# Kernel tuning notes

Hardware: AMD Instinct MI355X
Metric: run time of the kernel (lower is better)

Reference implementation:

```python
import jax, jax.numpy as jnp
import numpy as np

B, K, D = 16384, 64, 128


def setup_inputs() -> dict:
    key = jax.random.key(0)
    kx, kc = jax.random.split(key)
    x = jax.random.normal(kx, (B, D), dtype=jnp.float32)
    centers = jax.random.uniform(kc, (K, D), dtype=jnp.float32)  # torch.rand init
    return {"x": x, "centers": centers}


def reference(x, centers):
    batch, dim = x.shape
    k = centers.shape[0]
    # pairwise squared distances, same math as sum((x - c)^2)
    diff = x[:, None, :] - centers[None, :, :]          # [B, K, D]
    dist_sq = jnp.sum(diff * diff, axis=-1)             # [B, K]
    expo = -0.5 * dist_sq
    # safe softmax over clusters (identical to max-subtracted exp/sum)
    resp = jax.nn.softmax(expo, axis=-1)                # [B, K]
    log_resp = jnp.log(jnp.clip(resp, 1e-8))
    # hard assignment and per-cluster statistics
    assign = jnp.argmin(dist_sq, axis=-1)               # [B] int
    onehot = jax.nn.one_hot(assign, k, dtype=x.dtype)   # [B, K]
    cluster_weight = jnp.sum(onehot, axis=0)            # [K]
    emp_total = jnp.einsum('nk,nd->kd', onehot, x)      # [K, D]
    emp_mean = emp_total / (cluster_weight[:, None] + 1e-7)
    # masked centered samples: onehot[n,k]*(x_n - mean_k) is nonzero only at k=assign(n)
    xm = x - emp_mean[assign]                           # [B, D]
    covar_total = jnp.einsum('nk,nd,ne->kde', onehot, xm, xm)  # [K, D, D]
    covar = covar_total / (cluster_weight[:, None, None] + 1e-7)
    eye = jnp.eye(dim, dtype=x.dtype)
    covar_diag = covar * eye
    covar_off = covar * (1.0 - eye)
    diag_dist_sq = jnp.sum((covar_diag - eye) ** 2, axis=(1, 2))  # [K]
    off_dist_sq = jnp.sum(covar_off ** 2, axis=(1, 2))            # [K]
    mean_dist_sq = jnp.sum((emp_mean - centers) ** 2, axis=1)     # [K]
    mean_mse = jnp.sum(cluster_weight * mean_dist_sq) / (batch * dim)
    covar_mse = jnp.sum(
        cluster_weight * diag_dist_sq / (batch * dim)
        + cluster_weight * off_dist_sq / (batch * dim * (dim - 1.0))
    )
    return log_resp, mean_mse, covar_mse
```

## Files before the change

kernel.cpp:

```cpp
#include <hip/hip_runtime.h>

#define BB 16384
#define KK 64
#define DD 128
#define SEG 128
#define MAXITEMS 192
#define NRB 4
#define RSLAB 4096
#define RBLKS (KK * NRB)

typedef __attribute__((ext_vector_type(8))) short bf16x8;
typedef __attribute__((ext_vector_type(4))) float f32x4;

__device__ __forceinline__ unsigned int packbf2(float a, float b) {
    unsigned ua = __float_as_uint(a);
    unsigned ub = __float_as_uint(b);
    ua = (ua + 0x7FFFu + ((ua >> 16) & 1u)) >> 16;
    ub = (ub + 0x7FFFu + ((ub >> 16) & 1u)) >> 16;
    return ua | (ub << 16);
}

__global__ __launch_bounds__(512) void k_rows(
    const float* __restrict__ x, const float* __restrict__ centers,
    float* __restrict__ log_resp, int* __restrict__ assign,
    int* __restrict__ bhist, int* __restrict__ counter)
{
    __shared__ float xs[64][132];
    __shared__ float ct[DD][66];
    __shared__ float cn2[KK];
    __shared__ int   lh[KK];

    const int tid = threadIdx.x;
    const int row0 = blockIdx.x * 64;

    if (blockIdx.x == 0 && tid == 0) *counter = 0;
    if (tid < KK) lh[tid] = 0;

    for (int g = tid; g < 64 * 32; g += 512) {
        int r = g >> 5, c4 = g & 31;
        float4 v = ((const float4*)(x + (size_t)(row0 + r) * DD))[c4];
        *(float4*)&xs[r][c4 * 4] = v;
    }
    for (int g = tid; g < KK * 32; g += 512) {
        int k = g >> 5, c4 = g & 31;
        float4 v = ((const float4*)(centers + (size_t)k * DD))[c4];
        ct[c4 * 4 + 0][k] = v.x;
        ct[c4 * 4 + 1][k] = v.y;
        ct[c4 * 4 + 2][k] = v.z;
        ct[c4 * 4 + 3][k] = v.w;
    }
    __syncthreads();
    if (tid < KK) {
        float s = 0.f;
        for (int d = 0; d < DD; ++d) { float c = ct[d][tid]; s = fmaf(c, c, s); }
        cn2[tid] = s;
    }
    __syncthreads();

    const int tr = tid >> 5;
    const int tc = tid & 31;
    const int k0 = tc * 2, k1 = k0 + 1;

    float acc0[4], acc1[4];
    #pragma unroll
    for (int i = 0; i < 4; ++i) { acc0[i] = 0.f; acc1[i] = 0.f; }

    for (int d = 0; d < DD; d += 4) {
        float2 b0 = *(const float2*)&ct[d + 0][k0];
        float2 b1 = *(const float2*)&ct[d + 1][k0];
        float2 b2 = *(const float2*)&ct[d + 2][k0];
        float2 b3 = *(const float2*)&ct[d + 3][k0];
        #pragma unroll
        for (int i = 0; i < 4; ++i) {
            float4 a = *(const float4*)&xs[tr * 4 + i][d];
            acc0[i] = fmaf(a.x, b0.x, acc0[i]);
            acc1[i] = fmaf(a.x, b0.y, acc1[i]);
            acc0[i] = fmaf(a.y, b1.x, acc0[i]);
            acc1[i] = fmaf(a.y, b1.y, acc1[i]);
            acc0[i] = fmaf(a.z, b2.x, acc0[i]);
            acc1[i] = fmaf(a.z, b2.y, acc1[i]);
            acc0[i] = fmaf(a.w, b3.x, acc0[i]);
            acc1[i] = fmaf(a.w, b3.y, acc1[i]);
        }
    }

    const float cn0 = 0.5f * cn2[k0], cn1 = 0.5f * cn2[k1];
    #pragma unroll
    for (int i = 0; i < 4; ++i) {
        int row = row0 + tr * 4 + i;
        float v0 = acc0[i] - cn0;
        float v1 = acc1[i] - cn1;
        float m; int idx;
        if (v1 > v0) { m = v1; idx = k1; } else { m = v0; idx = k0; }
        #pragma unroll
        for (int off = 1; off < 32; off <<= 1) {
            float ov = __shfl_xor(m, off);
            int   oi = __shfl_xor(idx, off);
            if (ov > m || (ov == m && oi < idx)) { m = ov; idx = oi; }
        }
        float s = expf(v0 - m) + expf(v1 - m);
        #pragma unroll
        for (int off = 1; off < 32; off <<= 1) s += __shfl_xor(s, off);
        float ls = logf(s);
        float lr0 = fmaxf(v0 - m - ls, -18.4206807f);
        float lr1 = fmaxf(v1 - m - ls, -18.4206807f);
        *(float2*)&log_resp[(size_t)row * KK + k0] = make_float2(lr0, lr1);
        if (tc == 0) {
            assign[row] = idx;
            atomicAdd(&lh[idx], 1);
        }
    }
    __syncthreads();
    if (tid < KK) bhist[blockIdx.x * KK + tid] = lh[tid];
}

__global__ __launch_bounds__(256) void k_scat(
    const int* __restrict__ assign, const int* __restrict__ bhist,
    int* __restrict__ sorted, float* __restrict__ cw,
    int4* __restrict__ items, int* __restrict__ item_count,
    int* __restrict__ ist, int* __restrict__ ien)
{
    __shared__ int ph_tot[4][KK], ph_pre[4][KK];
    __shared__ int cnt_s[KK], pre_s[KK], base_s[KK], cur_s[KK];
    __shared__ int iof[KK + 1];

    const int tid = threadIdx.x;
    const int b = blockIdx.x;
    const int t = tid & 63, q = tid >> 6;

    int tot = 0, pre = 0;
    const int bb0 = q * 64;
    for (int bb = bb0; bb < bb0 + 64; ++bb) {
        int v = bhist[bb * KK + t];
        tot += v;
        if (bb < b) pre += v;
    }
    ph_tot[q][t] = tot; ph_pre[q][t] = pre;
    __syncthreads();

    if (tid < KK) {
        cnt_s[tid] = ph_tot[0][tid] + ph_tot[1][tid] + ph_tot[2][tid] + ph_tot[3][tid];
        pre_s[tid] = ph_pre[0][tid] + ph_pre[1][tid] + ph_pre[2][tid] + ph_pre[3][tid];
        cur_s[tid] = 0;
    }
    __syncthreads();
    if (tid == 0) {
        int base = 0;
        for (int k = 0; k < KK; ++k) { base_s[k] = base; base += cnt_s[k]; }
    }
    __syncthreads();

    if (tid < 64) {
        int r = b * 64 + tid;
        int a = assign[r];
        int p = base_s[a] + pre_s[a] + atomicAdd(&cur_s[a], 1);
        sorted[p] = r;
    }

    if (b == 0) {
        if (tid < KK) cw[tid] = (float)cnt_s[tid];
        if (tid == 0) {
            int ic = 0;
            for (int k = 0; k < KK; ++k) {
                iof[k] = ic;
                ic += (cnt_s[k] + SEG - 1) / SEG;
            }
            iof[KK] = ic;
            *item_count = ic;
        }
        __syncthreads();
        if (tid < KK) {
            const int k = tid, c = cnt_s[k], io = iof[k];
            ist[k] = io;
            ien[k] = iof[k + 1];
            int j = 0;
            for (int s = 0; s < c; s += SEG, ++j) {
                int4 it; it.x = k; it.y = base_s[k] + s;
                it.z = min(SEG, c - s); it.w = 0;
                items[io + j] = it;
            }
        }
    }
}

__global__ __launch_bounds__(256) void k_seg(
    const float* __restrict__ x, const int* __restrict__ sorted,
    const int4* __restrict__ items, const int* __restrict__ item_count,
    float* __restrict__ part, float* __restrict__ emp_part)
{
    if ((int)blockIdx.x >= *item_count) return;
    int4 it = items[blockIdx.x];
    const int gstart = it.y, len = it.z;

    __shared__ int rows_s[128];
    __shared__ unsigned int XT[DD][68];

    const int tid = threadIdx.x;
    const int w = tid >> 6, lane = tid & 63;
    const int c4 = lane & 15, q = lane >> 4;

    f32x4 acc[2][8];
    #pragma unroll
    for (int h = 0; h < 2; ++h)
        #pragma unroll
        for (int nt = 0; nt < 8; ++nt)
            acc[h][nt] = (f32x4){0.f, 0.f, 0.f, 0.f};
    float colsum = 0.f;

    for (int half = 0; half < 2; ++half) {
        const int hoff = half * 128;
        const int hlen = min(128, len - hoff);
        if (hlen <= 0) break;

        __syncthreads();
        if (tid < hlen) rows_s[tid] = sorted[gstart + hoff + tid];
        __syncthreads();

        {
            const int r0 = 2 * lane, r1 = 2 * lane + 1;
            const int d0 = w * 32;
            const float* p0 = x + (size_t)rows_s[r0 < hlen ? r0 : 0] * DD + d0;
            const float* p1 = x + (size_t)rows_s[r1 < hlen ? r1 : 0] * DD + d0;
            #pragma unroll
            for (int i = 0; i < 8; ++i) {
                float4 a = make_float4(0.f, 0.f, 0.f, 0.f);
                float4 b = make_float4(0.f, 0.f, 0.f, 0.f);
                if (r0 < hlen) a = *(const float4*)(p0 + 4 * i);
                if (r1 < hlen) b = *(const float4*)(p1 + 4 * i);
                XT[d0 + 4 * i + 0][lane] = packbf2(a.x, b.x);
                XT[d0 + 4 * i + 1][lane] = packbf2(a.y, b.y);
                XT[d0 + 4 * i + 2][lane] = packbf2(a.z, b.z);
                XT[d0 + 4 * i + 3][lane] = packbf2(a.w, b.w);
            }
        }
        __syncthreads();

        if (tid < DD) {
            float s = 0.f;
            #pragma unroll
            for (int j4 = 0; j4 < 16; ++j4) {
                uint4 v = *(const uint4*)&XT[tid][j4 * 4];
                s += __uint_as_float(v.x << 16) + __uint_as_float(v.x & 0xFFFF0000u);
                s += __uint_as_float(v.y << 16) + __uint_as_float(v.y & 0xFFFF0000u);
                s += __uint_as_float(v.z << 16) + __uint_as_float(v.z & 0xFFFF0000u);
                s += __uint_as_float(v.w << 16) + __uint_as_float(v.w & 0xFFFF0000u);
            }
            colsum += s;
        }

        #pragma unroll
        for (int c = 0; c < 4; ++c) {
            const int ku = c * 16 + q * 4;
            bf16x8 a0 = *(const bf16x8*)&XT[(2 * w + 0) * 16 + c4][ku];
            bf16x8 a1 = *(const bf16x8*)&XT[(2 * w + 1) * 16 + c4][ku];
            #pragma unroll
            for (int nt = 0; nt < 8; ++nt) {
                bf16x8 b = *(const bf16x8*)&XT[nt * 16 + c4][ku];
                acc[0][nt] = __builtin_amdgcn_mfma_f32_16x16x32_bf16(a0, b, acc[0][nt], 0, 0, 0);
                acc[1][nt] = __builtin_amdgcn_mfma_f32_16x16x32_bf16(a1, b, acc[1][nt], 0, 0, 0);
            }
        }
    }

    if (tid < DD) emp_part[blockIdx.x * DD + tid] = colsum;

    float* pb = part + (size_t)blockIdx.x * (DD * DD);
    #pragma unroll
    for (int h = 0; h < 2; ++h) {
        const int m0 = (2 * w + h) * 16 + q * 4;
        #pragma unroll
        for (int nt = 0; nt < 8; ++nt) {
            const int n = nt * 16 + c4;
            pb[(m0 + 0) * DD + n] = acc[h][nt].x;
            pb[(m0 + 1) * DD + n] = acc[h][nt].y;
            pb[(m0 + 2) * DD + n] = acc[h][nt].z;
            pb[(m0 + 3) * DD + n] = acc[h][nt].w;
        }
    }
}

__global__ __launch_bounds__(256) void k_redfinal(
    const float* __restrict__ part, const float* __restrict__ emp_part,
    const float* __restrict__ cw, const float* __restrict__ centers,
    const int* __restrict__ ist, const int* __restrict__ ien,
    float2* __restrict__ spart, int* __restrict__ counter,
    float* __restrict__ outscalars)
{
    const int k = blockIdx.x >> 2;
    const int p = blockIdx.x & 3;
    const int i0 = ist[k], i1 = ien[k];
    const int tid = threadIdx.x;
    const int w = tid >> 6, lane = tid & 63;
    const float wgt = cw[k];
    const float inv = 1.0f / (wgt + 1e-7f);

    __shared__ float mu_s[DD], emp_s[DD];
    __shared__ float emp2[2][DD];
    __shared__ float red[4][RSLAB];

    {
        const int dh = tid & 127, hf = tid >> 7;
        float e0 = 0.f, e1 = 0.f;
        int it = i0 + hf;
        for (; it + 2 < i1; it += 4) {
            e0 += emp_part[it * DD + dh];
            e1 += emp_part[(it + 2) * DD + dh];
        }
        if (it < i1) e0 += emp_part[it * DD + dh];
        emp2[hf][dh] = e0 + e1;
    }
    __syncthreads();
    if (tid < DD) {
        float e = emp2[0][tid] + emp2[1][tid];
        emp_s[tid] = e;
        mu_s[tid] = e * inv;
    }

    float4 acc[16];
    #pragma unroll
    for (int c = 0; c < 16; ++c) acc[c] = make_float4(0.f, 0.f, 0.f, 0.f);

    const int base = p * RSLAB;
    for (int it = i0 + w; it < i1; it += 4) {
        const float* pb = part + (size_t)it * (DD * DD) + base;
        #pragma unroll
        for (int c = 0; c < 16; ++c) {
            float4 v = *(const float4*)&pb[c * 256 + lane * 4];
            acc[c].x += v.x; acc[c].y += v.y; acc[c].z += v.z; acc[c].w += v.w;
        }
    }
    #pragma unroll
    for (int c = 0; c < 16; ++c)
        *(float4*)&red[w][c * 256 + lane * 4] = acc[c];
    __syncthreads();

    float ds = 0.f, os = 0.f, mm = 0.f;
    #pragma unroll
    for (int jj = 0; jj < 16; ++jj) {
        int el = jj * 256 + tid;
        float sx = red[0][el] + red[1][el] + red[2][el] + red[3][el];
        int gel = base + el;
        int d = gel >> 7, e = gel & 127;
        float ctv = sx - mu_s[d] * emp_s[e] - emp_s[d] * mu_s[e]
                  + wgt * mu_s[d] * mu_s[e];
        float v = ctv * inv;
        if (d == e) { float t = v - 1.f; ds += t * t; }
        else        { os += v * v; }
    }
    if (p == 0 && tid < DD) {
        float t = mu_s[tid] - centers[k * DD + tid];
        mm = t * t;
    }

    #pragma unroll
    for (int off = 32; off > 0; off >>= 1) {
        ds += __shfl_down(ds, off);
        os += __shfl_down(os, off);
        mm += __shfl_down(mm, off);
    }
    __shared__ float rds[4], ros[4], rmm[4];
    __shared__ int is_last;
    if (lane == 0) { rds[w] = ds; ros[w] = os; rmm[w] = mm; }
    __syncthreads();
    if (tid == 0) {
        float DS = rds[0] + rds[1] + rds[2] + rds[3];
        float OS = ros[0] + ros[1] + ros[2] + ros[3];
        float MM = rmm[0] + rmm[1] + rmm[2] + rmm[3];
        const float bd = (float)BB * (float)DD;
        float2 mine;
        mine.x = wgt * MM / bd;
        mine.y = wgt * DS / bd + wgt * OS / (bd * (float)(DD - 1));
        spart[blockIdx.x] = mine;
        __threadfence();
        int old = atomicAdd(counter, 1);
        is_last = (old == RBLKS - 1);
    }
    __syncthreads();
    if (is_last) {
        __threadfence();
        float2 v = (tid < RBLKS) ? spart[tid] : make_float2(0.f, 0.f);
        float a = v.x, b = v.y;
        #pragma unroll
        for (int off = 32; off > 0; off >>= 1) {
            a += __shfl_down(a, off);
            b += __shfl_down(b, off);
        }
        __shared__ float ra[4], rb[4];
        if (lane == 0) { ra[w] = a; rb[w] = b; }
        __syncthreads();
        if (tid == 0) {
            outscalars[0] = ra[0] + ra[1] + ra[2] + ra[3];
            outscalars[1] = rb[0] + rb[1] + rb[2] + rb[3];
        }
    }
}

extern "C" void kernel_launch(void* const* d_in, const int* in_sizes, int n_in,
                              void* d_out, int out_size, void* d_ws, size_t ws_size,
                              hipStream_t stream) {
    const float* x = (const float*)d_in[0];
    const float* centers = (const float*)d_in[1];
    float* out = (float*)d_out;
    float* outscalars = out + (size_t)BB * KK;

    char* ws = (char*)d_ws;
    size_t off = 0;
    float*  part     = (float*)(ws + off); off += (size_t)MAXITEMS * DD * DD * 4;
    float*  emp_part = (float*)(ws + off); off += (size_t)MAXITEMS * DD * 4;
    int*    sorted   = (int*)  (ws + off); off += BB * 4;
    int*    assign   = (int*)  (ws + off); off += BB * 4;
    int*    bhist    = (int*)  (ws + off); off += 256 * KK * 4;
    int4*   items    = (int4*) (ws + off); off += 256 * 16;
    float*  cw       = (float*)(ws + off); off += 256;
    int*    itemcnt  = (int*)  (ws + off); off += 256;
    int*    ist      = (int*)  (ws + off); off += 256;
    int*    ien      = (int*)  (ws + off); off += 256;
    float2* spart    = (float2*)(ws + off); off += RBLKS * 8;
    int*    counter  = (int*)  (ws + off); off += 256;

    k_rows    <<<256, 512, 0, stream>>>(x, centers, out, assign, bhist, counter);
    k_scat    <<<256, 256, 0, stream>>>(assign, bhist, sorted, cw, items,
                                        itemcnt, ist, ien);
    k_seg     <<<MAXITEMS, 256, 0, stream>>>(x, sorted, items, itemcnt,
                                             part, emp_part);
    k_redfinal<<<RBLKS, 256, 0, stream>>>(part, emp_part, cw, centers, ist, ien,
                                          spart, counter, outscalars);
}
```

Measured before the change: 113.5 us.

## Fuse segment covariance and reduction kernels with per-cluster arrival counters

Merges the segment Gram-matrix kernel and the per-cluster reduction kernel into one launch. Reducer blocks spin-wait on a per-cluster arrival counter set by producer blocks, which removes a kernel boundary and lets a cluster's reduction start once its own segments finish. Segments now hold at most 128 rows, so the two-half loop is dropped, and shared memory is unioned between the two roles. The cost is reducer blocks occupying CUs while they spin, with deadlock risk if the producers cannot be scheduled.

Result: slower. 158.9 us (+40.0%).

```diff
diff --git a/kernel.cpp b/kernel.cpp
--- a/kernel.cpp
+++ b/kernel.cpp
@@ -23,7 +23,7 @@
 __global__ __launch_bounds__(512) void k_rows(
     const float* __restrict__ x, const float* __restrict__ centers,
     float* __restrict__ log_resp, int* __restrict__ assign,
-    int* __restrict__ bhist, int* __restrict__ counter)
+    int* __restrict__ bhist)
 {
     __shared__ float xs[64][132];
     __shared__ float ct[DD][66];
@@ -33,7 +33,6 @@
     const int tid = threadIdx.x;
     const int row0 = blockIdx.x * 64;
 
-    if (blockIdx.x == 0 && tid == 0) *counter = 0;
     if (tid < KK) lh[tid] = 0;
 
     for (int g = tid; g < 64 * 32; g += 512) {
@@ -118,7 +117,8 @@
     const int* __restrict__ assign, const int* __restrict__ bhist,
     int* __restrict__ sorted, float* __restrict__ cw,
     int4* __restrict__ items, int* __restrict__ item_count,
-    int* __restrict__ ist, int* __restrict__ ien)
+    int* __restrict__ ist, int* __restrict__ ien,
+    int* __restrict__ arrived, int* __restrict__ counter)
 {
     __shared__ int ph_tot[4][KK], ph_pre[4][KK];
     __shared__ int cnt_s[KK], pre_s[KK], base_s[KK], cur_s[KK];
@@ -158,7 +158,11 @@
     }
 
     if (b == 0) {
-        if (tid < KK) cw[tid] = (float)cnt_s[tid];
+        if (tid < KK) {
+            cw[tid] = (float)cnt_s[tid];
+            arrived[tid] = 0;
+        }
+        if (tid == KK) *counter = 0;
         if (tid == 0) {
             int ic = 0;
             for (int k = 0; k < KK; ++k) {
@@ -183,120 +187,129 @@
     }
 }
 
-__global__ __launch_bounds__(256) void k_seg(
+struct PSmem {
+    int rows_s[128];
+    unsigned int XT[DD][68];
+};
+struct RSmem {
+    float red[4][RSLAB];
+    float mu_s[DD], emp_s[DD];
+    float emp2[2][DD];
+    float rds[4], ros[4], rmm[4];
+    float ra[4], rb[4];
+    int is_last;
+};
+union USmem { PSmem pr; RSmem rd; };
+
+__global__ __launch_bounds__(256) void k_segred(
     const float* __restrict__ x, const int* __restrict__ sorted,
     const int4* __restrict__ items, const int* __restrict__ item_count,
-    float* __restrict__ part, float* __restrict__ emp_part)
+    const int* __restrict__ ist, const int* __restrict__ ien,
+    const float* __restrict__ cw, const float* __restrict__ centers,
+    float* __restrict__ part, float* __restrict__ emp_part,
+    int* arrived, float2* __restrict__ spart,
+    int* __restrict__ counter, float* __restrict__ outscalars)
 {
-    if ((int)blockIdx.x >= *item_count) return;
-    int4 it = items[blockIdx.x];
-    const int gstart = it.y, len = it.z;
-
-    __shared__ int rows_s[128];
-    __shared__ unsigned int XT[DD][68];
-
+    __shared__ USmem sm;
     const int tid = threadIdx.x;
     const int w = tid >> 6, lane = tid & 63;
-    const int c4 = lane & 15, q = lane >> 4;
-
-    f32x4 acc[2][8];
-    #pragma unroll
-    for (int h = 0; h < 2; ++h)
-        #pragma unroll
-        for (int nt = 0; nt < 8; ++nt)
-            acc[h][nt] = (f32x4){0.f, 0.f, 0.f, 0.f};
-    float colsum = 0.f;
-
-    for (int half = 0; half < 2; ++half) {
-        const int hoff = half * 128;
-        const int hlen = min(128, len - hoff);
-        if (hlen <= 0) break;
-
-        __syncthreads();
-        if (tid < hlen) rows_s[tid] = sorted[gstart + hoff + tid];
+
+    if ((int)blockIdx.x < MAXITEMS) {
+        if ((int)blockIdx.x >= *item_count) return;
+        int4 it = items[blockIdx.x];
+        const int k = it.x, gstart = it.y, len = it.z;
+
+        const int c4 = lane & 15, q = lane >> 4;
+
+        f32x4 acc[2][8];
+        #pragma unroll
+        for (int h = 0; h < 2; ++h)
+            #pragma unroll
+            for (int nt = 0; nt < 8; ++nt)
+                acc[h][nt] = (f32x4){0.f, 0.f, 0.f, 0.f};
+
+        if (tid < len) sm.pr.rows_s[tid] = sorted[gstart + tid];
         __syncthreads();
 
         {
             const int r0 = 2 * lane, r1 = 2 * lane + 1;
             const int d0 = w * 32;
-            const float* p0 = x + (size_t)rows_s[r0 < hlen ? r0 : 0] * DD + d0;
-            const float* p1 = x + (size_t)rows_s[r1 < hlen ? r1 : 0] * DD + d0;
+            const float* p0 = x + (size_t)sm.pr.rows_s[r0 < len ? r0 : 0] * DD + d0;
+            const float* p1 = x + (size_t)sm.pr.rows_s[r1 < len ? r1 : 0] * DD + d0;
             #pragma unroll
             for (int i = 0; i < 8; ++i) {
                 float4 a = make_float4(0.f, 0.f, 0.f, 0.f);
                 float4 b = make_float4(0.f, 0.f, 0.f, 0.f);
-                if (r0 < hlen) a = *(const float4*)(p0 + 4 * i);
-                if (r1 < hlen) b = *(const float4*)(p1 + 4 * i);
-                XT[d0 + 4 * i + 0][lane] = packbf2(a.x, b.x);
-                XT[d0 + 4 * i + 1][lane] = packbf2(a.y, b.y);
-                XT[d0 + 4 * i + 2][lane] = packbf2(a.z, b.z);
-                XT[d0 + 4 * i + 3][lane] = packbf2(a.w, b.w);
+                if (r0 < len) a = *(const float4*)(p0 + 4 * i);
+                if (r1 < len) b = *(const float4*)(p1 + 4 * i);
+                sm.pr.XT[d0 + 4 * i + 0][lane] = packbf2(a.x, b.x);
+                sm.pr.XT[d0 + 4 * i + 1][lane] = packbf2(a.y, b.y);
+                sm.pr.XT[d0 + 4 * i + 2][lane] = packbf2(a.z, b.z);
+                sm.pr.XT[d0 + 4 * i + 3][lane] = packbf2(a.w, b.w);
             }
         }
         __syncthreads();
 
         if (tid < DD) {
-            float s = 0.f;
+            float colsum = 0.f;
             #pragma unroll
             for (int j4 = 0; j4 < 16; ++j4) {
-                uint4 v = *(const uint4*)&XT[tid][j4 * 4];
-                s += __uint_as_float(v.x << 16) + __uint_as_float(v.x & 0xFFFF0000u);
-                s += __uint_as_float(v.y << 16) + __uint_as_float(v.y & 0xFFFF0000u);
-                s += __uint_as_float(v.z << 16) + __uint_as_float(v.z & 0xFFFF0000u);
-                s += __uint_as_float(v.w << 16) + __uint_as_float(v.w & 0xFFFF0000u);
-            }
-            colsum += s;
+                uint4 v = *(const uint4*)&sm.pr.XT[tid][j4 * 4];
+                colsum += __uint_as_float(v.x << 16) + __uint_as_float(v.x & 0xFFFF0000u);
+                colsum += __uint_as_float(v.y << 16) + __uint_as_float(v.y & 0xFFFF0000u);
+                colsum += __uint_as_float(v.z << 16) + __uint_as_float(v.z & 0xFFFF0000u);
+                colsum += __uint_as_float(v.w << 16) + __uint_as_float(v.w & 0xFFFF0000u);
+            }
+            emp_part[blockIdx.x * DD + tid] = colsum;
         }
 
         #pragma unroll
         for (int c = 0; c < 4; ++c) {
             const int ku = c * 16 + q * 4;
-            bf16x8 a0 = *(const bf16x8*)&XT[(2 * w + 0) * 16 + c4][ku];
-            bf16x8 a1 = *(const bf16x8*)&XT[(2 * w + 1) * 16 + c4][ku];
+            bf16x8 a0 = *(const bf16x8*)&sm.pr.XT[(2 * w + 0) * 16 + c4][ku];
+            bf16x8 a1 = *(const bf16x8*)&sm.pr.XT[(2 * w + 1) * 16 + c4][ku];
             #pragma unroll
             for (int nt = 0; nt < 8; ++nt) {
-                bf16x8 b = *(const bf16x8*)&XT[nt * 16 + c4][ku];
+                bf16x8 b = *(const bf16x8*)&sm.pr.XT[nt * 16 + c4][ku];
                 acc[0][nt] = __builtin_amdgcn_mfma_f32_16x16x32_bf16(a0, b, acc[0][nt], 0, 0, 0);
                 acc[1][nt] = __builtin_amdgcn_mfma_f32_16x16x32_bf16(a1, b, acc[1][nt], 0, 0, 0);
             }
         }
-    }
-
-    if (tid < DD) emp_part[blockIdx.x * DD + tid] = colsum;
-
-    float* pb = part + (size_t)blockIdx.x * (DD * DD);
-    #pragma unroll
-    for (int h = 0; h < 2; ++h) {
-        const int m0 = (2 * w + h) * 16 + q * 4;
-        #pragma unroll
-        for (int nt = 0; nt < 8; ++nt) {
-            const int n = nt * 16 + c4;
-            pb[(m0 + 0) * DD + n] = acc[h][nt].x;
-            pb[(m0 + 1) * DD + n] = acc[h][nt].y;
-            pb[(m0 + 2) * DD + n] = acc[h][nt].z;
-            pb[(m0 + 3) * DD + n] = acc[h][nt].w;
-        }
-    }
-}
-
-__global__ __launch_bounds__(256) void k_redfinal(
-    const float* __restrict__ part, const float* __restrict__ emp_part,
-    const float* __restrict__ cw, const float* __restrict__ centers,
-    const int* __restrict__ ist, const int* __restrict__ ien,
-    float2* __restrict__ spart, int* __restrict__ counter,
-    float* __restrict__ outscalars)
-{
-    const int k = blockIdx.x >> 2;
-    const int p = blockIdx.x & 3;
+
+        float* pb = part + (size_t)blockIdx.x * (DD * DD);
+        #pragma unroll
+        for (int h = 0; h < 2; ++h) {
+            const int m0 = (2 * w + h) * 16 + q * 4;
+            #pragma unroll
+            for (int nt = 0; nt < 8; ++nt) {
+                const int n = nt * 16 + c4;
+                pb[(m0 + 0) * DD + n] = acc[h][nt].x;
+                pb[(m0 + 1) * DD + n] = acc[h][nt].y;
+                pb[(m0 + 2) * DD + n] = acc[h][nt].z;
+                pb[(m0 + 3) * DD + n] = acc[h][nt].w;
+            }
+        }
+
+        __threadfence();
+        __syncthreads();
+        if (tid == 0) atomicAdd(&arrived[k], 1);
+        return;
+    }
+
+    const int j = (int)blockIdx.x - MAXITEMS;
+    const int k = j >> 2;
+    const int p = j & 3;
     const int i0 = ist[k], i1 = ien[k];
-    const int tid = threadIdx.x;
-    const int w = tid >> 6, lane = tid & 63;
+    const int nitems = i1 - i0;
     const float wgt = cw[k];
     const float inv = 1.0f / (wgt + 1e-7f);
 
-    __shared__ float mu_s[DD], emp_s[DD];
-    __shared__ float emp2[2][DD];
-    __shared__ float red[4][RSLAB];
+    if (tid == 0 && nitems > 0) {
+        while (atomicAdd(&arrived[k], 0) < nitems)
+            __builtin_amdgcn_s_sleep(8);
+    }
+    __syncthreads();
+    __threadfence();
 
     {
         const int dh = tid & 127, hf = tid >> 7;
@@ -307,13 +320,13 @@
             e1 += emp_part[(it + 2) * DD + dh];
         }
         if (it < i1) e0 += emp_part[it * DD + dh];
-        emp2[hf][dh] = e0 + e1;
+        sm.rd.emp2[hf][dh] = e0 + e1;
     }
     __syncthreads();
     if (tid < DD) {
-        float e = emp2[0][tid] + emp2[1][tid];
-        emp_s[tid] = e;
-        mu_s[tid] = e * inv;
+        float e = sm.rd.emp2[0][tid] + sm.rd.emp2[1][tid];
+        sm.rd.emp_s[tid] = e;
+        sm.rd.mu_s[tid] = e * inv;
     }
 
     float4 acc[16];
@@ -331,24 +344,26 @@
     }
     #pragma unroll
     for (int c = 0; c < 16; ++c)
-        *(float4*)&red[w][c * 256 + lane * 4] = acc[c];
+        *(float4*)&sm.rd.red[w][c * 256 + lane * 4] = acc[c];
     __syncthreads();
 
     float ds = 0.f, os = 0.f, mm = 0.f;
     #pragma unroll
     for (int jj = 0; jj < 16; ++jj) {
         int el = jj * 256 + tid;
-        float sx = red[0][el] + red[1][el] + red[2][el] + red[3][el];
+        float sx = sm.rd.red[0][el] + sm.rd.red[1][el]
+                 + sm.rd.red[2][el] + sm.rd.red[3][el];
         int gel = base + el;
         int d = gel >> 7, e = gel & 127;
-        float ctv = sx - mu_s[d] * emp_s[e] - emp_s[d] * mu_s[e]
-                  + wgt * mu_s[d] * mu_s[e];
+        float ctv = sx - sm.rd.mu_s[d] * sm.rd.emp_s[e]
+                  - sm.rd.emp_s[d] * sm.rd.mu_s[e]
+                  + wgt * sm.rd.mu_s[d] * sm.rd.mu_s[e];
         float v = ctv * inv;
         if (d == e) { float t = v - 1.f; ds += t * t; }
         else        { os += v * v; }
     }
     if (p == 0 && tid < DD) {
-        float t = mu_s[tid] - centers[k * DD + tid];
+        float t = sm.rd.mu_s[tid] - centers[k * DD + tid];
         mm = t * t;
     }
 
@@ -358,25 +373,23 @@
         os += __shfl_down(os, off);
         mm += __shfl_down(mm, off);
     }
-    __shared__ float rds[4], ros[4], rmm[4];
-    __shared__ int is_last;
-    if (lane == 0) { rds[w] = ds; ros[w] = os; rmm[w] = mm; }
+    if (lane == 0) { sm.rd.rds[w] = ds; sm.rd.ros[w] = os; sm.rd.rmm[w] = mm; }
     __syncthreads();
     if (tid == 0) {
-        float DS = rds[0] + rds[1] + rds[2] + rds[3];
-        float OS = ros[0] + ros[1] + ros[2] + ros[3];
-        float MM = rmm[0] + rmm[1] + rmm[2] + rmm[3];
+        float DS = sm.rd.rds[0] + sm.rd.rds[1] + sm.rd.rds[2] + sm.rd.rds[3];
+        float OS = sm.rd.ros[0] + sm.rd.ros[1] + sm.rd.ros[2] + sm.rd.ros[3];
+        float MM = sm.rd.rmm[0] + sm.rd.rmm[1] + sm.rd.rmm[2] + sm.rd.rmm[3];
         const float bd = (float)BB * (float)DD;
         float2 mine;
         mine.x = wgt * MM / bd;
         mine.y = wgt * DS / bd + wgt * OS / (bd * (float)(DD - 1));
-        spart[blockIdx.x] = mine;
+        spart[j] = mine;
         __threadfence();
         int old = atomicAdd(counter, 1);
-        is_last = (old == RBLKS - 1);
-    }
-    __syncthreads();
-    if (is_last) {
+        sm.rd.is_last = (old == RBLKS - 1);
+    }
+    __syncthreads();
+    if (sm.rd.is_last) {
         __threadfence();
         float2 v = (tid < RBLKS) ? spart[tid] : make_float2(0.f, 0.f);
         float a = v.x, b = v.y;
@@ -385,12 +398,11 @@
             a += __shfl_down(a, off);
             b += __shfl_down(b, off);
         }
-        __shared__ float ra[4], rb[4];
-        if (lane == 0) { ra[w] = a; rb[w] = b; }
+        if (lane == 0) { sm.rd.ra[w] = a; sm.rd.rb[w] = b; }
         __syncthreads();
         if (tid == 0) {
-            outscalars[0] = ra[0] + ra[1] + ra[2] + ra[3];
-            outscalars[1] = rb[0] + rb[1] + rb[2] + rb[3];
+            outscalars[0] = sm.rd.ra[0] + sm.rd.ra[1] + sm.rd.ra[2] + sm.rd.ra[3];
+            outscalars[1] = sm.rd.rb[0] + sm.rd.rb[1] + sm.rd.rb[2] + sm.rd.rb[3];
         }
     }
 }
@@ -415,14 +427,14 @@
     int*    itemcnt  = (int*)  (ws + off); off += 256;
     int*    ist      = (int*)  (ws + off); off += 256;
     int*    ien      = (int*)  (ws + off); off += 256;
+    int*    arrived  = (int*)  (ws + off); off += KK * 4;
     float2* spart    = (float2*)(ws + off); off += RBLKS * 8;
     int*    counter  = (int*)  (ws + off); off += 256;
 
-    k_rows    <<<256, 512, 0, stream>>>(x, centers, out, assign, bhist, counter);
-    k_scat    <<<256, 256, 0, stream>>>(assign, bhist, sorted, cw, items,
-                                        itemcnt, ist, ien);
-    k_seg     <<<MAXITEMS, 256, 0, stream>>>(x, sorted, items, itemcnt,
-                                             part, emp_part);
-    k_redfinal<<<RBLKS, 256, 0, stream>>>(part, emp_part, cw, centers, ist, ien,
-                                          spart, counter, outscalars);
+    k_rows  <<<256, 512, 0, stream>>>(x, centers, out, assign, bhist);
+    k_scat  <<<256, 256, 0, stream>>>(assign, bhist, sorted, cw, items,
+                                      itemcnt, ist, ien, arrived, counter);
+    k_segred<<<MAXITEMS + RBLKS, 256, 0, stream>>>(
+        x, sorted, items, itemcnt, ist, ien, cw, centers,
+        part, emp_part, arrived, spart, counter, outscalars);
 }
```

## Compute row-center dot products with split-bf16 MFMA in k_rows

Applied to the files above, without the earlier changes.

Replaces the scalar FP32 FMA dot-product loop in k_rows with bf16 MFMA 16x16x32 instructions. Each operand is split into a high and a low bf16 part, and three MFMAs per tile keep close to FP32 accuracy. The block shrinks to 256 threads (4 waves, each covering 16 rows by 64 centers), and the softmax/argmin reductions now shuffle across 16 lanes. The aim is to cut the FP32 ALU cost of the distance GEMM. The cost is split-conversion work during loading and a small precision risk for argmin ties.

Result: no change. 111.4 us, median of 2 (-1.9%).

```diff
diff --git a/kernel.cpp b/kernel.cpp
--- a/kernel.cpp
+++ b/kernel.cpp
@@ -20,14 +20,30 @@
     return ua | (ub << 16);
 }
 
-__global__ __launch_bounds__(512) void k_rows(
+__device__ __forceinline__ unsigned bf16rne(float f) {
+    unsigned u = __float_as_uint(f);
+    return (u + 0x7FFFu + ((u >> 16) & 1u)) >> 16;
+}
+__device__ __forceinline__ float bf16tof(unsigned h) {
+    return __uint_as_float(h << 16);
+}
+__device__ __forceinline__ void split4(float4 v, uint2& hi, uint2& lo) {
+    unsigned hx = bf16rne(v.x), hy = bf16rne(v.y);
+    unsigned hz = bf16rne(v.z), hw = bf16rne(v.w);
+    hi.x = hx | (hy << 16); hi.y = hz | (hw << 16);
+    unsigned lx = bf16rne(v.x - bf16tof(hx)), ly = bf16rne(v.y - bf16tof(hy));
+    unsigned lz = bf16rne(v.z - bf16tof(hz)), lw = bf16rne(v.w - bf16tof(hw));
+    lo.x = lx | (ly << 16); lo.y = lz | (lw << 16);
+}
+
+__global__ __launch_bounds__(256) void k_rows(
     const float* __restrict__ x, const float* __restrict__ centers,
     float* __restrict__ log_resp, int* __restrict__ assign,
     int* __restrict__ bhist, int* __restrict__ counter)
 {
-    __shared__ float xs[64][132];
-    __shared__ float ct[DD][66];
-    __shared__ float cn2[KK];
+    __shared__ unsigned int XH[64][68], XLo[64][68];
+    __shared__ unsigned int CH[64][68], CLo[64][68];
+    __shared__ float cn2_s[KK];
     __shared__ int   lh[KK];
 
     const int tid = threadIdx.x;
@@ -36,76 +52,84 @@
     if (blockIdx.x == 0 && tid == 0) *counter = 0;
     if (tid < KK) lh[tid] = 0;
 
-    for (int g = tid; g < 64 * 32; g += 512) {
-        int r = g >> 5, c4 = g & 31;
-        float4 v = ((const float4*)(x + (size_t)(row0 + r) * DD))[c4];
-        *(float4*)&xs[r][c4 * 4] = v;
-    }
-    for (int g = tid; g < KK * 32; g += 512) {
-        int k = g >> 5, c4 = g & 31;
-        float4 v = ((const float4*)(centers + (size_t)k * DD))[c4];
-        ct[c4 * 4 + 0][k] = v.x;
-        ct[c4 * 4 + 1][k] = v.y;
-        ct[c4 * 4 + 2][k] = v.z;
-        ct[c4 * 4 + 3][k] = v.w;
-    }
-    __syncthreads();
+    for (int g = tid; g < 64 * 32; g += 256) {
+        int r = g >> 5, c4g = g & 31;
+        float4 v = ((const float4*)(x + (size_t)(row0 + r) * DD))[c4g];
+        uint2 hi, lo; split4(v, hi, lo);
+        *(uint2*)&XH[r][c4g * 2] = hi;
+        *(uint2*)&XLo[r][c4g * 2] = lo;
+    }
+    for (int g = tid; g < 64 * 32; g += 256) {
+        int k = g >> 5, c4g = g & 31;
+        float4 v = ((const float4*)(centers + (size_t)k * DD))[c4g];
+        uint2 hi, lo; split4(v, hi, lo);
+        *(uint2*)&CH[k][c4g * 2] = hi;
+        *(uint2*)&CLo[k][c4g * 2] = lo;
+    }
     if (tid < KK) {
         float s = 0.f;
-        for (int d = 0; d < DD; ++d) { float c = ct[d][tid]; s = fmaf(c, c, s); }
-        cn2[tid] = s;
-    }
-    __syncthreads();
-
-    const int tr = tid >> 5;
-    const int tc = tid & 31;
-    const int k0 = tc * 2, k1 = k0 + 1;
-
-    float acc0[4], acc1[4];
-    #pragma unroll
-    for (int i = 0; i < 4; ++i) { acc0[i] = 0.f; acc1[i] = 0.f; }
-
-    for (int d = 0; d < DD; d += 4) {
-        float2 b0 = *(const float2*)&ct[d + 0][k0];
-        float2 b1 = *(const float2*)&ct[d + 1][k0];
-        float2 b2 = *(const float2*)&ct[d + 2][k0];
-        float2 b3 = *(const float2*)&ct[d + 3][k0];
-        #pragma unroll
-        for (int i = 0; i < 4; ++i) {
-            float4 a = *(const float4*)&xs[tr * 4 + i][d];
-            acc0[i] = fmaf(a.x, b0.x, acc0[i]);
-            acc1[i] = fmaf(a.x, b0.y, acc1[i]);
-            acc0[i] = fmaf(a.y, b1.x, acc0[i]);
-            acc1[i] = fmaf(a.y, b1.y, acc1[i]);
-            acc0[i] = fmaf(a.z, b2.x, acc0[i]);
-            acc1[i] = fmaf(a.z, b2.y, acc1[i]);
-            acc0[i] = fmaf(a.w, b3.x, acc0[i]);
-            acc1[i] = fmaf(a.w, b3.y, acc1[i]);
-        }
-    }
-
-    const float cn0 = 0.5f * cn2[k0], cn1 = 0.5f * cn2[k1];
-    #pragma unroll
-    for (int i = 0; i < 4; ++i) {
-        int row = row0 + tr * 4 + i;
-        float v0 = acc0[i] - cn0;
-        float v1 = acc1[i] - cn1;
-        float m; int idx;
-        if (v1 > v0) { m = v1; idx = k1; } else { m = v0; idx = k0; }
-        #pragma unroll
-        for (int off = 1; off < 32; off <<= 1) {
+        const float4* cp = (const float4*)(centers + (size_t)tid * DD);
+        for (int c4g = 0; c4g < 32; ++c4g) {
+            float4 v = cp[c4g];
+            s = fmaf(v.x, v.x, s); s = fmaf(v.y, v.y, s);
+            s = fmaf(v.z, v.z, s); s = fmaf(v.w, v.w, s);
+        }
+        cn2_s[tid] = s;
+    }
+    __syncthreads();
+
+    const int w = tid >> 6, lane = tid & 63;
+    const int c4 = lane & 15, q = lane >> 4;
+
+    f32x4 acc[4];
+    #pragma unroll
+    for (int nt = 0; nt < 4; ++nt) acc[nt] = (f32x4){0.f, 0.f, 0.f, 0.f};
+
+    #pragma unroll
+    for (int c = 0; c < 4; ++c) {
+        const int ku = c * 16 + q * 4;
+        bf16x8 ah = *(const bf16x8*)&XH[w * 16 + c4][ku];
+        bf16x8 al = *(const bf16x8*)&XLo[w * 16 + c4][ku];
+        #pragma unroll
+        for (int nt = 0; nt < 4; ++nt) {
+            bf16x8 bh = *(const bf16x8*)&CH[nt * 16 + c4][ku];
+            bf16x8 bl = *(const bf16x8*)&CLo[nt * 16 + c4][ku];
+            acc[nt] = __builtin_amdgcn_mfma_f32_16x16x32_bf16(ah, bh, acc[nt], 0, 0, 0);
+            acc[nt] = __builtin_amdgcn_mfma_f32_16x16x32_bf16(ah, bl, acc[nt], 0, 0, 0);
+            acc[nt] = __builtin_amdgcn_mfma_f32_16x16x32_bf16(al, bh, acc[nt], 0, 0, 0);
+        }
+    }
+
+    float cn[4];
+    #pragma unroll
+    for (int nt = 0; nt < 4; ++nt) cn[nt] = 0.5f * cn2_s[nt * 16 + c4];
+
+    #pragma unroll
+    for (int j = 0; j < 4; ++j) {
+        const int row = row0 + w * 16 + q * 4 + j;
+        float v0 = acc[0][j] - cn[0];
+        float v1 = acc[1][j] - cn[1];
+        float v2 = acc[2][j] - cn[2];
+        float v3 = acc[3][j] - cn[3];
+        float m = v0; int idx = c4;
+        if (v1 > m) { m = v1; idx = 16 + c4; }
+        if (v2 > m) { m = v2; idx = 32 + c4; }
+        if (v3 > m) { m = v3; idx = 48 + c4; }
+        #pragma unroll
+        for (int off = 1; off < 16; off <<= 1) {
             float ov = __shfl_xor(m, off);
             int   oi = __shfl_xor(idx, off);
             if (ov > m || (ov == m && oi < idx)) { m = ov; idx = oi; }
         }
-        float s = expf(v0 - m) + expf(v1 - m);
-        #pragma unroll
-        for (int off = 1; off < 32; off <<= 1) s += __shfl_xor(s, off);
+        float s = expf(v0 - m) + expf(v1 - m) + expf(v2 - m) + expf(v3 - m);
+        #pragma unroll
+        for (int off = 1; off < 16; off <<= 1) s += __shfl_xor(s, off);
         float ls = logf(s);
-        float lr0 = fmaxf(v0 - m - ls, -18.4206807f);
-        float lr1 = fmaxf(v1 - m - ls, -18.4206807f);
-        *(float2*)&log_resp[(size_t)row * KK + k0] = make_float2(lr0, lr1);
-        if (tc == 0) {
+        log_resp[(size_t)row * KK +  0 + c4] = fmaxf(v0 - m - ls, -18.4206807f);
+        log_resp[(size_t)row * KK + 16 + c4] = fmaxf(v1 - m - ls, -18.4206807f);
+        log_resp[(size_t)row * KK + 32 + c4] = fmaxf(v2 - m - ls, -18.4206807f);
+        log_resp[(size_t)row * KK + 48 + c4] = fmaxf(v3 - m - ls, -18.4206807f);
+        if (c4 == 0) {
             assign[row] = idx;
             atomicAdd(&lh[idx], 1);
         }
@@ -418,7 +442,7 @@
     float2* spart    = (float2*)(ws + off); off += RBLKS * 8;
     int*    counter  = (int*)  (ws + off); off += 256;
 
-    k_rows    <<<256, 512, 0, stream>>>(x, centers, out, assign, bhist, counter);
+    k_rows    <<<256, 256, 0, stream>>>(x, centers, out, assign, bhist, counter);
     k_scat    <<<256, 256, 0, stream>>>(assign, bhist, sorted, cw, items,
                                         itemcnt, ist, ien);
     k_seg     <<<MAXITEMS, 256, 0, stream>>>(x, sorted, items, itemcnt,
```
